# Kernel tuning notes

Hardware: AMD Instinct MI355X
Metric: run time of the kernel (lower is better)

Reference implementation:

```python
import jax, jax.numpy as jnp
import numpy as np

LN_EPS = 1e-5  # torch nn.LayerNorm default


def setup_inputs() -> dict:
    key = jax.random.key(0)
    kx, kw = jax.random.split(key)
    tokens, d_in, d_out = 8192, 4096, 16384
    x = jax.random.normal(kx, (tokens, d_in), dtype=jnp.float32)
    # nn.Linear weight layout: [out_features, in_features]
    W = jax.random.normal(kw, (d_out, d_in), dtype=jnp.float32) * (1.0 / np.sqrt(d_in))
    return {"x": x, "W": W}


def reference(x, W):
    # LayerNorm over last dim, no affine params (elementwise_affine=False)
    mean = jnp.mean(x, axis=-1, keepdims=True)
    var = jnp.mean(jnp.square(x - mean), axis=-1, keepdims=True)  # biased, as torch LN
    xn = (x - mean) * jax.lax.rsqrt(var + LN_EPS)
    # Linear (no bias): [tokens, d_in] @ [d_in, d_out]
    y = jnp.einsum("td,od->to", xn, W)
    return jax.nn.sigmoid(y)
```

## Files before the change

kernel.cpp:

```cpp
#include <hip/hip_runtime.h>
#include <hip/hip_bf16.h>
#include <stdint.h>

#define TOKENS 8192
#define DIN    4096
#define DOUT   16384

#define BM 256
#define BN 256
#define BKT 64
#define NT (DIN / BKT)
#define NJ (NT / 2)

typedef short s16x8 __attribute__((ext_vector_type(8)));
typedef float f32x16 __attribute__((ext_vector_type(16)));

#define AS1 __attribute__((address_space(1)))
#define AS3 __attribute__((address_space(3)))
#define VMCNT(n)  asm volatile("s_waitcnt vmcnt(" #n ")" ::: "memory")
#define BAR()     __builtin_amdgcn_s_barrier()

__device__ __forceinline__ unsigned short f2bf(float f) {
  unsigned int u = __float_as_uint(f);
  u += 0x7fffu + ((u >> 16) & 1u);
  return (unsigned short)(u >> 16);
}

__global__ __launch_bounds__(256) void ln_kernel(const float* __restrict__ x,
                                                 unsigned short* __restrict__ xn) {
  const int row = blockIdx.x;
  const float4* xr = reinterpret_cast<const float4*>(x + (size_t)row * DIN);
  float4 v[4];
  float sum = 0.f, ssq = 0.f;
#pragma unroll
  for (int i = 0; i < 4; ++i) {
    v[i] = xr[threadIdx.x + i * 256];
    sum += v[i].x + v[i].y + v[i].z + v[i].w;
    ssq += v[i].x * v[i].x + v[i].y * v[i].y + v[i].z * v[i].z + v[i].w * v[i].w;
  }
#pragma unroll
  for (int off = 32; off > 0; off >>= 1) {
    sum += __shfl_xor(sum, off, 64);
    ssq += __shfl_xor(ssq, off, 64);
  }
  __shared__ float red[8];
  const int wid = threadIdx.x >> 6;
  if ((threadIdx.x & 63) == 0) { red[wid] = sum; red[wid + 4] = ssq; }
  __syncthreads();
  sum = red[0] + red[1] + red[2] + red[3];
  ssq = red[4] + red[5] + red[6] + red[7];
  const float mean = sum * (1.f / DIN);
  const float var  = ssq * (1.f / DIN) - mean * mean;
  const float rs   = rsqrtf(var + 1e-5f);
  ushort4* xo = reinterpret_cast<ushort4*>(xn + (size_t)row * DIN);
#pragma unroll
  for (int i = 0; i < 4; ++i) {
    ushort4 o;
    o.x = f2bf((v[i].x - mean) * rs);
    o.y = f2bf((v[i].y - mean) * rs);
    o.z = f2bf((v[i].z - mean) * rs);
    o.w = f2bf((v[i].w - mean) * rs);
    xo[threadIdx.x + i * 256] = o;
  }
}

__global__ __launch_bounds__(256) void cvt_kernel(const float* __restrict__ W,
                                                  unsigned short* __restrict__ Wb) {
  const size_t i = (size_t)blockIdx.x * 256 + threadIdx.x;
  float4 v = reinterpret_cast<const float4*>(W)[i];
  ushort4 o;
  o.x = f2bf(v.x); o.y = f2bf(v.y); o.z = f2bf(v.z); o.w = f2bf(v.w);
  reinterpret_cast<ushort4*>(Wb)[i] = o;
}

__global__ __launch_bounds__(512, 2) void gemm_sig(const unsigned short* __restrict__ A,
                                                   const unsigned short* __restrict__ B,
                                                   float* __restrict__ C) {
  __shared__ unsigned short Asl[2 * 256 * 64];
  __shared__ unsigned short Bsl[2 * 256 * 64];

  const int bid = blockIdx.x;
  const int cpx = gridDim.x >> 3;
  const int swz = (bid & 7) * cpx + (bid >> 3);
  const int grp = swz >> 2;
  const int sub = swz & 3;
  const int bm = ((grp & 15) << 1) | (sub & 1);
  const int bn = ((grp >> 4) << 1) | (sub >> 1);

  const int tid  = threadIdx.x;
  const int wid  = tid >> 6;
  const int lane = tid & 63;
  const int wr = wid >> 2, wc = wid & 3;

  const unsigned short* gA = A + (size_t)bm * BM * DIN;
  const unsigned short* gB = B + (size_t)bn * BN * DIN;

  const int l8 = lane >> 3, l7 = lane & 7;
  const int csw = l7 ^ l8;
  const unsigned short* sA = gA + (size_t)(wid * 8 + l8) * DIN + csw * 8;
  const unsigned short* sB = gB + (size_t)(wid * 8 + l8) * DIN + csw * 8;
  const int dOfs = wid * 512;

#define STG_Aq(p, q, kt) __builtin_amdgcn_global_load_lds( \
    (const AS1 void*)(sA + (size_t)(q) * 64 * DIN + (size_t)(kt) * BKT), \
    (AS3 void*)(Asl + ((p) * 256 + (q) * 64) * 64 + dOfs), 16, 0, 0)
#define STG_Bq(p, q, kt) __builtin_amdgcn_global_load_lds( \
    (const AS1 void*)(sB + (size_t)(q) * 64 * DIN + (size_t)(kt) * BKT), \
    (AS3 void*)(Bsl + ((p) * 256 + (q) * 64) * 64 + dOfs), 16, 0, 0)

  const int l31 = lane & 31;
  const int l5  = lane >> 5;
  int aRow[4], bRow[2], kslt[4];
#pragma unroll
  for (int mb = 0; mb < 4; ++mb) aRow[mb] = (wr * 128 + mb * 32 + l31) * 64;
#pragma unroll
  for (int nb = 0; nb < 2; ++nb) bRow[nb] = (wc * 64 + nb * 32 + l31) * 64;
#pragma unroll
  for (int ks = 0; ks < 4; ++ks) kslt[ks] = ((2 * ks + l5) ^ l7) * 8;

  s16x8 a0[4], a1[4], b0[4], b1[4];
  f32x16 acc[4][2] = {};

#define RD_AP(p, mp) do { _Pragma("unroll") for (int ks = 0; ks < 4; ++ks) { \
    a0[ks] = *reinterpret_cast<const s16x8*>(Asl + (p) * 16384 + aRow[2 * (mp)] + kslt[ks]); \
    a1[ks] = *reinterpret_cast<const s16x8*>(Asl + (p) * 16384 + aRow[2 * (mp) + 1] + kslt[ks]); } } while (0)
#define RD_BALL(p) do { _Pragma("unroll") for (int ks = 0; ks < 4; ++ks) { \
    b0[ks] = *reinterpret_cast<const s16x8*>(Bsl + (p) * 16384 + bRow[0] + kslt[ks]); \
    b1[ks] = *reinterpret_cast<const s16x8*>(Bsl + (p) * 16384 + bRow[1] + kslt[ks]); } } while (0)
#define MMPH(mp) do { _Pragma("unroll") for (int ks = 0; ks < 4; ++ks) { \
    acc[2 * (mp)][0]     = __builtin_amdgcn_mfma_f32_32x32x16_bf16(a0[ks], b0[ks], acc[2 * (mp)][0], 0, 0, 0); \
    acc[2 * (mp)][1]     = __builtin_amdgcn_mfma_f32_32x32x16_bf16(a0[ks], b1[ks], acc[2 * (mp)][1], 0, 0, 0); \
    acc[2 * (mp) + 1][0] = __builtin_amdgcn_mfma_f32_32x32x16_bf16(a1[ks], b0[ks], acc[2 * (mp) + 1][0], 0, 0, 0); \
    acc[2 * (mp) + 1][1] = __builtin_amdgcn_mfma_f32_32x32x16_bf16(a1[ks], b1[ks], acc[2 * (mp) + 1][1], 0, 0, 0); } } while (0)

  STG_Aq(0, 0, 0); STG_Aq(0, 1, 0); STG_Aq(0, 2, 0); STG_Aq(0, 3, 0);
  STG_Bq(0, 0, 0); STG_Bq(0, 1, 0); STG_Bq(0, 2, 0); STG_Bq(0, 3, 0);
  STG_Bq(1, 0, 1); STG_Bq(1, 1, 1); STG_Bq(1, 2, 1); STG_Bq(1, 3, 1);
  VMCNT(4); BAR();

  for (int j = 0; j < NJ - 1; ++j) {
    const int t1 = 2 * j + 1, t2 = 2 * j + 2, t3 = 2 * j + 3;
    VMCNT(4);
    RD_AP(0, 0); RD_BALL(0);
    STG_Aq(1, 0, t1); STG_Aq(1, 1, t1); STG_Aq(1, 2, t1); STG_Aq(1, 3, t1);
    MMPH(0); BAR();
    RD_AP(0, 1);
    STG_Aq(0, 0, t2); STG_Aq(0, 2, t2); STG_Bq(0, 0, t2); STG_Bq(0, 1, t2);
    MMPH(1); BAR();
    VMCNT(4);
    RD_AP(1, 0); RD_BALL(1);
    STG_Bq(0, 2, t2); STG_Bq(0, 3, t2); STG_Aq(0, 1, t2); STG_Aq(0, 3, t2);
    MMPH(0); BAR();
    RD_AP(1, 1);
    STG_Bq(1, 0, t3); STG_Bq(1, 1, t3); STG_Bq(1, 2, t3); STG_Bq(1, 3, t3);
    MMPH(1); BAR();
  }

  {
    const int t1 = NT - 1;
    VMCNT(4);
    RD_AP(0, 0); RD_BALL(0);
    STG_Aq(1, 0, t1); STG_Aq(1, 1, t1); STG_Aq(1, 2, t1); STG_Aq(1, 3, t1);
    MMPH(0); BAR();
    RD_AP(0, 1);
    MMPH(1); BAR();
    VMCNT(0);
    RD_AP(1, 0); RD_BALL(1);
    MMPH(0); BAR();
    RD_AP(1, 1);
    MMPH(1); BAR();
  }

#undef STG_Aq
#undef STG_Bq
#undef RD_AP
#undef RD_BALL
#undef MMPH

  const int crow0 = bm * BM + wr * 128 + 4 * l5;
  const int ccol0 = bn * BN + wc * 64 + l31;
#pragma unroll
  for (int mb = 0; mb < 4; ++mb)
#pragma unroll
    for (int nb = 0; nb < 2; ++nb)
#pragma unroll
      for (int reg = 0; reg < 16; ++reg) {
        const int r = crow0 + mb * 32 + (reg & 3) + 8 * (reg >> 2);
        const int c = ccol0 + nb * 32;
        const float v = acc[mb][nb][reg];
        C[(size_t)r * DOUT + c] = 1.f / (1.f + __expf(-v));
      }
}

extern "C" void kernel_launch(void* const* d_in, const int* in_sizes, int n_in,
                              void* d_out, int out_size, void* d_ws, size_t ws_size,
                              hipStream_t stream) {
  const float* x = (const float*)d_in[0];
  const float* W = (const float*)d_in[1];
  float* out = (float*)d_out;

  unsigned short* xn = (unsigned short*)d_ws;
  unsigned short* Wb = xn + (size_t)TOKENS * DIN;

  ln_kernel<<<TOKENS, 256, 0, stream>>>(x, xn);
  cvt_kernel<<<((size_t)DOUT * DIN) / 1024, 256, 0, stream>>>(W, Wb);
  gemm_sig<<<(TOKENS / BM) * (DOUT / BN), 512, 0, stream>>>(xn, Wb, out);
}
```

Measured before the change: 1.139 ms.

## Double-buffer B fragments in registers and restage global-to-LDS schedule

Adds a second register set for B fragments (bX/bY) so B for the next K-tile is read from LDS one phase early, overlapping the LDS reads with MFMA work. Global-to-LDS staging is regrouped into whole-A and whole-B tile loads with a vmcnt wait in every phase. This doubles B fragment register usage, which risks spilling or lowering occupancy at launch_bounds(512,2), and the reordered waits may change how well memory latency is hidden.

```diff
diff --git a/kernel.cpp b/kernel.cpp
--- a/kernel.cpp
+++ b/kernel.cpp
@@ -101,12 +101,14 @@
   const unsigned short* sB = gB + (size_t)(wid * 8 + l8) * DIN + csw * 8;
   const int dOfs = wid * 512;
 
-#define STG_Aq(p, q, kt) __builtin_amdgcn_global_load_lds( \
-    (const AS1 void*)(sA + (size_t)(q) * 64 * DIN + (size_t)(kt) * BKT), \
-    (AS3 void*)(Asl + ((p) * 256 + (q) * 64) * 64 + dOfs), 16, 0, 0)
-#define STG_Bq(p, q, kt) __builtin_amdgcn_global_load_lds( \
-    (const AS1 void*)(sB + (size_t)(q) * 64 * DIN + (size_t)(kt) * BKT), \
-    (AS3 void*)(Bsl + ((p) * 256 + (q) * 64) * 64 + dOfs), 16, 0, 0)
+#define STG_A(p, kt) do { _Pragma("unroll") for (int q = 0; q < 4; ++q) \
+  __builtin_amdgcn_global_load_lds( \
+    (const AS1 void*)(sA + (size_t)q * 64 * DIN + (size_t)(kt) * BKT), \
+    (AS3 void*)(Asl + ((p) * 256 + q * 64) * 64 + dOfs), 16, 0, 0); } while (0)
+#define STG_B(p, kt) do { _Pragma("unroll") for (int q = 0; q < 4; ++q) \
+  __builtin_amdgcn_global_load_lds( \
+    (const AS1 void*)(sB + (size_t)q * 64 * DIN + (size_t)(kt) * BKT), \
+    (AS3 void*)(Bsl + ((p) * 256 + q * 64) * 64 + dOfs), 16, 0, 0); } while (0)
 
   const int l31 = lane & 31;
   const int l5  = lane >> 5;
@@ -118,63 +120,65 @@
 #pragma unroll
   for (int ks = 0; ks < 4; ++ks) kslt[ks] = ((2 * ks + l5) ^ l7) * 8;
 
-  s16x8 a0[4], a1[4], b0[4], b1[4];
+  s16x8 a0[4], a1[4], bX[8], bY[8];
   f32x16 acc[4][2] = {};
 
 #define RD_AP(p, mp) do { _Pragma("unroll") for (int ks = 0; ks < 4; ++ks) { \
     a0[ks] = *reinterpret_cast<const s16x8*>(Asl + (p) * 16384 + aRow[2 * (mp)] + kslt[ks]); \
     a1[ks] = *reinterpret_cast<const s16x8*>(Asl + (p) * 16384 + aRow[2 * (mp) + 1] + kslt[ks]); } } while (0)
-#define RD_BALL(p) do { _Pragma("unroll") for (int ks = 0; ks < 4; ++ks) { \
-    b0[ks] = *reinterpret_cast<const s16x8*>(Bsl + (p) * 16384 + bRow[0] + kslt[ks]); \
-    b1[ks] = *reinterpret_cast<const s16x8*>(Bsl + (p) * 16384 + bRow[1] + kslt[ks]); } } while (0)
-#define MMPH(mp) do { _Pragma("unroll") for (int ks = 0; ks < 4; ++ks) { \
-    acc[2 * (mp)][0]     = __builtin_amdgcn_mfma_f32_32x32x16_bf16(a0[ks], b0[ks], acc[2 * (mp)][0], 0, 0, 0); \
-    acc[2 * (mp)][1]     = __builtin_amdgcn_mfma_f32_32x32x16_bf16(a0[ks], b1[ks], acc[2 * (mp)][1], 0, 0, 0); \
-    acc[2 * (mp) + 1][0] = __builtin_amdgcn_mfma_f32_32x32x16_bf16(a1[ks], b0[ks], acc[2 * (mp) + 1][0], 0, 0, 0); \
-    acc[2 * (mp) + 1][1] = __builtin_amdgcn_mfma_f32_32x32x16_bf16(a1[ks], b1[ks], acc[2 * (mp) + 1][1], 0, 0, 0); } } while (0)
-
-  STG_Aq(0, 0, 0); STG_Aq(0, 1, 0); STG_Aq(0, 2, 0); STG_Aq(0, 3, 0);
-  STG_Bq(0, 0, 0); STG_Bq(0, 1, 0); STG_Bq(0, 2, 0); STG_Bq(0, 3, 0);
-  STG_Bq(1, 0, 1); STG_Bq(1, 1, 1); STG_Bq(1, 2, 1); STG_Bq(1, 3, 1);
+#define RD_BPRE(p, dst) do { _Pragma("unroll") for (int ks = 0; ks < 4; ++ks) { \
+    dst[ks]     = *reinterpret_cast<const s16x8*>(Bsl + (p) * 16384 + bRow[0] + kslt[ks]); \
+    dst[4 + ks] = *reinterpret_cast<const s16x8*>(Bsl + (p) * 16384 + bRow[1] + kslt[ks]); } } while (0)
+#define MMPH(mp, bArr) do { _Pragma("unroll") for (int ks = 0; ks < 4; ++ks) { \
+    acc[2 * (mp)][0]     = __builtin_amdgcn_mfma_f32_32x32x16_bf16(a0[ks], bArr[ks],     acc[2 * (mp)][0], 0, 0, 0); \
+    acc[2 * (mp)][1]     = __builtin_amdgcn_mfma_f32_32x32x16_bf16(a0[ks], bArr[4 + ks], acc[2 * (mp)][1], 0, 0, 0); \
+    acc[2 * (mp) + 1][0] = __builtin_amdgcn_mfma_f32_32x32x16_bf16(a1[ks], bArr[ks],     acc[2 * (mp) + 1][0], 0, 0, 0); \
+    acc[2 * (mp) + 1][1] = __builtin_amdgcn_mfma_f32_32x32x16_bf16(a1[ks], bArr[4 + ks], acc[2 * (mp) + 1][1], 0, 0, 0); } } while (0)
+
+  STG_B(0, 0); STG_A(0, 0); STG_B(1, 1);
   VMCNT(4); BAR();
+  RD_BPRE(0, bX);
 
   for (int j = 0; j < NJ - 1; ++j) {
     const int t1 = 2 * j + 1, t2 = 2 * j + 2, t3 = 2 * j + 3;
     VMCNT(4);
-    RD_AP(0, 0); RD_BALL(0);
-    STG_Aq(1, 0, t1); STG_Aq(1, 1, t1); STG_Aq(1, 2, t1); STG_Aq(1, 3, t1);
-    MMPH(0); BAR();
-    RD_AP(0, 1);
-    STG_Aq(0, 0, t2); STG_Aq(0, 2, t2); STG_Bq(0, 0, t2); STG_Bq(0, 1, t2);
-    MMPH(1); BAR();
-    VMCNT(4);
-    RD_AP(1, 0); RD_BALL(1);
-    STG_Bq(0, 2, t2); STG_Bq(0, 3, t2); STG_Aq(0, 1, t2); STG_Aq(0, 3, t2);
-    MMPH(0); BAR();
-    RD_AP(1, 1);
-    STG_Bq(1, 0, t3); STG_Bq(1, 1, t3); STG_Bq(1, 2, t3); STG_Bq(1, 3, t3);
-    MMPH(1); BAR();
+    RD_AP(0, 0);
+    STG_A(1, t1);
+    MMPH(0, bX); BAR();
+    VMCNT(4);
+    RD_AP(0, 1); RD_BPRE(1, bY);
+    STG_B(0, t2);
+    MMPH(1, bX); BAR();
+    VMCNT(4);
+    RD_AP(1, 0);
+    STG_A(0, t2);
+    MMPH(0, bY); BAR();
+    VMCNT(4);
+    RD_AP(1, 1); RD_BPRE(0, bX);
+    STG_B(1, t3);
+    MMPH(1, bY); BAR();
   }
 
   {
     const int t1 = NT - 1;
     VMCNT(4);
-    RD_AP(0, 0); RD_BALL(0);
-    STG_Aq(1, 0, t1); STG_Aq(1, 1, t1); STG_Aq(1, 2, t1); STG_Aq(1, 3, t1);
-    MMPH(0); BAR();
-    RD_AP(0, 1);
-    MMPH(1); BAR();
+    RD_AP(0, 0);
+    STG_A(1, t1);
+    MMPH(0, bX); BAR();
+    VMCNT(4);
+    RD_AP(0, 1); RD_BPRE(1, bY);
+    MMPH(1, bX); BAR();
     VMCNT(0);
-    RD_AP(1, 0); RD_BALL(1);
-    MMPH(0); BAR();
+    RD_AP(1, 0);
+    MMPH(0, bY); BAR();
     RD_AP(1, 1);
-    MMPH(1); BAR();
-  }
-
-#undef STG_Aq
-#undef STG_Bq
+    MMPH(1, bY); BAR();
+  }
+
+#undef STG_A
+#undef STG_B
 #undef RD_AP
-#undef RD_BALL
+#undef RD_BPRE
 #undef MMPH
 
   const int crow0 = bm * BM + wr * 128 + 4 * l5;
```

Result: no change. 1.155 ms (+1.4%).
